# Kernel tuning notes

Hardware: AMD Instinct MI355X
Metric: run time of the kernel (lower is better)

## Reference

```python
import jax, jax.numpy as jnp
import numpy as np

N_NODES = 50000
N_EDGES = 1250000
D_IN = 64
D_HID = 64
D_OUT = 16
N_GRAPHS = 128


def setup_inputs() -> dict:
    key = jax.random.key(0)
    ks = jax.random.split(key, 16)
    glorot = lambda k, shape: jax.random.normal(k, shape, jnp.float32) * (2.0 / (shape[0] + shape[1])) ** 0.5
    inp = {
        "x": jax.random.normal(ks[0], (N_NODES, D_IN), jnp.float32),
        "edge_index": jax.random.randint(ks[1], (2, N_EDGES), 0, N_NODES, jnp.int32),
        "adj": jnp.zeros((1,), jnp.float32),
        "batch": jnp.sort(jax.random.randint(ks[2], (N_NODES,), 0, N_GRAPHS, jnp.int32)),
        # GraphConv layer 1: lin_rel (with bias) on aggregated msgs, lin_root (no bias) on x
        "W_rel1": glorot(ks[3], (D_IN, D_HID)),
        "b_rel1": jnp.zeros((D_HID,), jnp.float32),
        "W_root1": glorot(ks[4], (D_IN, D_HID)),
        "W_rel2": glorot(ks[5], (D_HID, D_HID)),
        "b_rel2": jnp.zeros((D_HID,), jnp.float32),
        "W_root2": glorot(ks[6], (D_HID, D_HID)),
        "W_rel3": glorot(ks[7], (D_HID, D_HID)),
        "b_rel3": jnp.zeros((D_HID,), jnp.float32),
        "W_root3": glorot(ks[8], (D_HID, D_HID)),
        "W_lin": glorot(ks[9], (D_HID, D_OUT)),
        "b_lin": jnp.zeros((D_OUT,), jnp.float32),
    }
    return inp


def graph_conv(x, src, dst, W_rel, b_rel, W_root):
    # PyG GraphConv (aggr='add'): out[i] = (sum_{j->i} x[j]) @ W_rel + b_rel + x[i] @ W_root
    agg = jax.ops.segment_sum(x[src], dst, num_segments=N_NODES)  # [N, d]
    return agg @ W_rel + b_rel + x @ W_root


def reference(x, edge_index, adj, batch,
              W_rel1, b_rel1, W_root1,
              W_rel2, b_rel2, W_root2,
              W_rel3, b_rel3, W_root3,
              W_lin, b_lin):
    src, dst = edge_index[0], edge_index[1]
    h = jax.nn.relu(graph_conv(x, src, dst, W_rel1, b_rel1, W_root1))
    h = jax.nn.relu(graph_conv(h, src, dst, W_rel2, b_rel2, W_root2))
    h = graph_conv(h, src, dst, W_rel3, b_rel3, W_root3)
    # global_mean_pool over batch ids
    sums = jax.ops.segment_sum(h, batch, num_segments=N_GRAPHS)  # [G, d]
    counts = jax.ops.segment_sum(jnp.ones((h.shape[0],), h.dtype), batch, num_segments=N_GRAPHS)
    pooled = sums / jnp.maximum(counts, 1.0)[:, None]
    return pooled @ W_lin + b_lin  # [G, D_OUT]
```

## Files before the change

### kernel.cpp

```cpp
#include <hip/hip_runtime.h>

#define D 64
#define N_GRAPHS 128
#define D_OUT 16
#define BCAP 16384
#define TILE 4096
#define ECAP 2048

typedef unsigned short u16;
typedef unsigned int u32;
typedef unsigned char u8;
typedef __attribute__((ext_vector_type(8))) short bf16x8;
typedef __attribute__((ext_vector_type(4))) float f32x4;
typedef __attribute__((ext_vector_type(2))) float f32x2;

__device__ inline u16 f2bf(float f) {
  u32 u = __float_as_uint(f);
  return (u16)((u + 0x7fffu + ((u >> 16) & 1u)) >> 16);
}
__device__ inline float bf2f(u16 b) { return __uint_as_float((u32)b << 16); }
__device__ inline f32x2 bfpair(u32 v) {
  return (f32x2){__uint_as_float(v << 16), __uint_as_float(v & 0xffff0000u)};
}

__global__ __launch_bounds__(256) void cvtbin_kernel(
    const float* __restrict__ xin, u16* __restrict__ hX, int n4, int nbin,
    const int* __restrict__ src, const int* __restrict__ dst,
    int* __restrict__ cursors, u32* __restrict__ binned, int n_edges, int nbuck,
    const float* __restrict__ Wrel1, const float* __restrict__ Wroot1,
    const float* __restrict__ Wrel2, const float* __restrict__ Wroot2,
    const float* __restrict__ Wrel3, const float* __restrict__ Wroot3,
    const float* __restrict__ Wlin, const float* __restrict__ brel3,
    const float* __restrict__ blin,
    float* __restrict__ M1, float* __restrict__ M2, float* __restrict__ cvec,
    u16* __restrict__ WbT1r, u16* __restrict__ WbT1o,
    u16* __restrict__ WbT2r, u16* __restrict__ WbT2o) {
  __shared__ u32 ent[TILE];
  __shared__ u8 ebk[TILE];
  __shared__ int hist[256];
  __shared__ int startb[256];
  __shared__ int cur[256];
  __shared__ int gbase[256];
  int t = threadIdx.x;

  if ((int)blockIdx.x < nbin) {
    hist[t] = 0;
    __syncthreads();
    int base = blockIdx.x * TILE;
    int cnt = n_edges - base;
    if (cnt > TILE) cnt = TILE;

    int mys[16], myd[16];
#pragma unroll
    for (int j = 0; j < 16; j++) {
      int i = base + t + j * 256;
      if (t + j * 256 < cnt) {
        mys[j] = src[i];
        myd[j] = dst[i];
        atomicAdd(&hist[myd[j] >> 8], 1);
      } else {
        myd[j] = -1;
      }
    }
    __syncthreads();
    int myc = hist[t];
    for (int off = 1; off < 256; off <<= 1) {
      int tmp = (t >= off) ? hist[t - off] : 0;
      __syncthreads();
      hist[t] += tmp;
      __syncthreads();
    }
    int excl = hist[t] - myc;
    startb[t] = excl;
    cur[t] = excl;
    __syncthreads();

#pragma unroll
    for (int j = 0; j < 16; j++) {
      if (myd[j] >= 0) {
        int b = myd[j] >> 8;
        int p = atomicAdd(&cur[b], 1);
        ent[p] = ((u32)myd[j] << 16) | (u32)mys[j];
        ebk[p] = (u8)b;
      }
    }
    __syncthreads();

    if (t < nbuck && myc > 0) gbase[t] = atomicAdd(&cursors[t], myc);
    __syncthreads();

#pragma unroll
    for (int j = 0; j < 16; j++) {
      int p = t + j * 256;
      if (p < cnt) {
        int b = ebk[p];
        int gpos = gbase[b] + (p - startb[b]);
        if (gpos < BCAP) binned[(size_t)b * BCAP + gpos] = ent[p];
      }
    }
    return;
  }

  int cb = blockIdx.x - nbin;
  if (cb == 0) {
    if (t >= 240) {
      int o = t - 240;
      float c = blin[o];
#pragma unroll
      for (int j = 0; j < D; j++) c = fmaf(brel3[j], Wlin[j * D_OUT + o], c);
      cvec[o] = c;
    }
  } else if (cb <= 8) {
    int idx = (cb - 1) * 256 + t;
    const float* W = (idx < 1024) ? Wrel3 : Wroot3;
    float* M = (idx < 1024) ? M1 : M2;
    int id = idx & 1023;
    int k = id >> 4, o = id & 15;
    float acc = 0.0f;
#pragma unroll
    for (int j = 0; j < D; j++) acc = fmaf(W[k * D + j], Wlin[j * D_OUT + o], acc);
    M[id] = acc;
  } else if (cb <= 16) {
    int tid = (cb - 9) * 256 + t;
    int mat = tid >> 9;
    int r = tid & 511;
    int o = r >> 3;
    int k0 = (r & 7) * 8;
    const float* Wsrc = (mat == 0) ? Wrel1 : (mat == 1) ? Wroot1
                       : (mat == 2) ? Wrel2 : Wroot2;
    u16* Wdst = (mat == 0) ? WbT1r : (mat == 1) ? WbT1o
               : (mat == 2) ? WbT2r : WbT2o;
    u16 tmp[8];
#pragma unroll
    for (int j = 0; j < 8; j++) tmp[j] = f2bf(Wsrc[(k0 + j) * D + o]);
    uint4 pw;
    pw.x = (u32)tmp[0] | ((u32)tmp[1] << 16);
    pw.y = (u32)tmp[2] | ((u32)tmp[3] << 16);
    pw.z = (u32)tmp[4] | ((u32)tmp[5] << 16);
    pw.w = (u32)tmp[6] | ((u32)tmp[7] << 16);
    *(uint4*)&Wdst[o * D + k0] = pw;
  }
  int i = cb * 256 + t;
  if (i >= n4) return;
  float4 v = ((const float4*)xin)[i];
  ushort4 o4;
  o4.x = f2bf(v.x); o4.y = f2bf(v.y); o4.z = f2bf(v.z); o4.w = f2bf(v.w);
  ((ushort4*)hX)[i] = o4;
}

__global__ __launch_bounds__(256) void csr_kernel(
    const u32* __restrict__ binned, const int* __restrict__ cursors,
    u16* __restrict__ csr_src, int* __restrict__ offsets,
    int n_nodes, int nbuck) {
  __shared__ int deg[256];
  __shared__ int cur[256];
  __shared__ int red[256];
  __shared__ u16 lcsr[BCAP];
  int b = blockIdx.x, t = threadIdx.x;
  int cnt = cursors[b];
  if (cnt < 0) cnt = 0;
  if (cnt > BCAP) cnt = BCAP;

  int c = 0;
  if (t < b) {
    c = cursors[t];
    if (c < 0) c = 0;
    if (c > BCAP) c = BCAP;
  }
  red[t] = c;
  __syncthreads();
  for (int off = 128; off > 0; off >>= 1) {
    if (t < off) red[t] += red[t + off];
    __syncthreads();
  }
  int ebase = red[0];

  int nodeBase = b << 8;
  int nn = n_nodes - nodeBase;
  if (nn > 256) nn = 256;

  deg[t] = 0;
  __syncthreads();
  const u32* be = binned + (size_t)b * BCAP;
  for (int i = t; i < cnt; i += 256)
    atomicAdd(&deg[(be[i] >> 16) - nodeBase], 1);
  __syncthreads();
  int myd = deg[t];
  for (int off = 1; off < 256; off <<= 1) {
    int tmp = (t >= off) ? deg[t - off] : 0;
    __syncthreads();
    deg[t] += tmp;
    __syncthreads();
  }
  int loff = deg[t] - myd;
  cur[t] = loff;
  if (t < nn) offsets[nodeBase + t] = ebase + loff;
  if (b == nbuck - 1 && t == 0) offsets[n_nodes] = ebase + cnt;
  __syncthreads();

  for (int i = t; i < cnt; i += 256) {
    u32 e = be[i];
    int ln = (e >> 16) - nodeBase;
    int p = atomicAdd(&cur[ln], 1);
    lcsr[p] = (u16)(e & 0xffffu);
  }
  __syncthreads();
  for (int i = t; i < cnt; i += 256) csr_src[ebase + i] = lcsr[i];
}

#define ACC8(a, r) \
  a[0] += bfpair(r.x); a[1] += bfpair(r.y); a[2] += bfpair(r.z); a[3] += bfpair(r.w);

#define GATHER_PROLOGUE(soff, permAr, eidx, blockBase, n_nodes, offsets, csr_src, gsrc, ebase0, scnt) \
  {                                                                     \
    int t_ = threadIdx.x;                                               \
    if (t_ < 33) {                                                      \
      int idx = blockBase + t_;                                         \
      if (idx > n_nodes) idx = n_nodes;                                 \
      soff[t_] = offsets[idx];                                          \
    }                                                                   \
    __syncthreads();                                                    \
    ebase0 = soff[0];                                                   \
    int ecnt_ = soff[32] - ebase0;                                      \
    scnt = ecnt_ < ECAP ? ecnt_ : ECAP;                                 \
    gsrc = csr_src + ebase0;                                            \
    if (t_ < 32) {                                                      \
      int d_ = (blockBase + t_ < n_nodes) ? soff[t_ + 1] - soff[t_] : -1; \
      int r_ = 0;                                                       \
      for (int j_ = 0; j_ < 32; j_++) {                                 \
        int dj_ = (blockBase + j_ < n_nodes) ? soff[j_ + 1] - soff[j_] : -1; \
        if (dj_ > d_ || (dj_ == d_ && j_ < t_)) r_++;                   \
      }                                                                 \
      permAr[r_] = (u8)t_;                                              \
    }                                                                   \
    for (int e_ = t_; e_ < scnt; e_ += 256) eidx[e_] = gsrc[e_];        \
    __syncthreads();                                                    \
  }

#define IDX(i) ((i) < ECAP ? (int)eidx[i] : (int)gsrc[i])

#define GATHER_LOOP(h, fo, ls, le, a0, a1)                                   \
  {                                                                          \
    int i = ls;                                                              \
    for (; i + 7 < le; i += 8) {                                             \
      int s0 = IDX(i),     s1 = IDX(i + 1), s2 = IDX(i + 2), s3 = IDX(i + 3);\
      int s4 = IDX(i + 4), s5 = IDX(i + 5), s6 = IDX(i + 6), s7 = IDX(i + 7);\
      uint4 r0 = *(const uint4*)(h + ((size_t)s0 << 6) + fo);                \
      uint4 r1 = *(const uint4*)(h + ((size_t)s1 << 6) + fo);                \
      uint4 r2 = *(const uint4*)(h + ((size_t)s2 << 6) + fo);                \
      uint4 r3 = *(const uint4*)(h + ((size_t)s3 << 6) + fo);                \
      uint4 r4 = *(const uint4*)(h + ((size_t)s4 << 6) + fo);                \
      uint4 r5 = *(const uint4*)(h + ((size_t)s5 << 6) + fo);                \
      uint4 r6 = *(const uint4*)(h + ((size_t)s6 << 6) + fo);                \
      uint4 r7 = *(const uint4*)(h + ((size_t)s7 << 6) + fo);                \
      ACC8(a0, r0) ACC8(a1, r1) ACC8(a0, r2) ACC8(a1, r3)                    \
      ACC8(a0, r4) ACC8(a1, r5) ACC8(a0, r6) ACC8(a1, r7)                    \
    }                                                                        \
    for (; i + 3 < le; i += 4) {                                             \
      int s0 = IDX(i), s1 = IDX(i + 1), s2 = IDX(i + 2), s3 = IDX(i + 3);    \
      uint4 r0 = *(const uint4*)(h + ((size_t)s0 << 6) + fo);                \
      uint4 r1 = *(const uint4*)(h + ((size_t)s1 << 6) + fo);                \
      uint4 r2 = *(const uint4*)(h + ((size_t)s2 << 6) + fo);                \
      uint4 r3 = *(const uint4*)(h + ((size_t)s3 << 6) + fo);                \
      ACC8(a0, r0) ACC8(a1, r1) ACC8(a0, r2) ACC8(a1, r3)                    \
    }                                                                        \
    for (; i < le; i++) {                                                    \
      int s0 = IDX(i);                                                       \
      uint4 r0 = *(const uint4*)(h + ((size_t)s0 << 6) + fo);                \
      ACC8(a0, r0)                                                           \
    }                                                                        \
  }

__global__ __launch_bounds__(256) void fused_layer_kernel(
    const u16* __restrict__ h, const int* __restrict__ offsets,
    const u16* __restrict__ csr_src,
    const u16* __restrict__ WbTrel, const u16* __restrict__ WbTroot,
    const float* __restrict__ brel,
    u16* __restrict__ h_out, int n_nodes, int do_relu) {
  __shared__ __align__(16) u16 ldsA[32 * 72];
  __shared__ __align__(16) u16 ldsX[32 * 72];
  __shared__ int soff[33];
  __shared__ u8 permAr[32];
  __shared__ u16 eidx[ECAP];
  int w = threadIdx.x >> 6;
  int lane = threadIdx.x & 63;
  int sub = lane >> 3;
  int fo = (lane & 7) * 8;
  int blockBase = blockIdx.x * 32;
  const u16* gsrc;
  int ebase0, scnt;

  GATHER_PROLOGUE(soff, permAr, eidx, blockBase, n_nodes, offsets, csr_src, gsrc, ebase0, scnt)

  int ln = permAr[w * 8 + sub];
  int node = blockBase + ln;
  bool valid = node < n_nodes;
  int ls = soff[ln] - ebase0;
  int le = soff[ln + 1] - ebase0;
  if (!valid) le = ls;
  int lrow = ln * 72;

  uint4 xr = make_uint4(0, 0, 0, 0);
  if (valid) xr = *(const uint4*)(h + ((size_t)node << 6) + fo);
  *(uint4*)&ldsX[lrow + fo] = xr;

  f32x2 a0[4] = {{0,0},{0,0},{0,0},{0,0}};
  f32x2 a1[4] = {{0,0},{0,0},{0,0},{0,0}};
  GATHER_LOOP(h, fo, ls, le, a0, a1)
#pragma unroll
  for (int k = 0; k < 4; k++) a0[k] += a1[k];

  uint4 pa;
  pa.x = (u32)f2bf(a0[0].x) | ((u32)f2bf(a0[0].y) << 16);
  pa.y = (u32)f2bf(a0[1].x) | ((u32)f2bf(a0[1].y) << 16);
  pa.z = (u32)f2bf(a0[2].x) | ((u32)f2bf(a0[2].y) << 16);
  pa.w = (u32)f2bf(a0[3].x) | ((u32)f2bf(a0[3].y) << 16);
  *(uint4*)&ldsA[lrow + fo] = pa;
  __syncthreads();

  int mt = w & 1;
  int ntb = (w >> 1) * 2;
  int lr = lane & 15, lk = lane >> 4;
  int arow = (mt * 16 + lr) * 72;
  bf16x8 af0 = *(const bf16x8*)&ldsA[arow + lk * 8];
  bf16x8 af1 = *(const bf16x8*)&ldsA[arow + 32 + lk * 8];
  bf16x8 xf0 = *(const bf16x8*)&ldsX[arow + lk * 8];
  bf16x8 xf1 = *(const bf16x8*)&ldsX[arow + 32 + lk * 8];
#pragma unroll
  for (int tt = 0; tt < 2; tt++) {
    int nt = ntb + tt;
    int wrow = (nt * 16 + lr) * D + lk * 8;
    bf16x8 br0 = *(const bf16x8*)(WbTrel + wrow);
    bf16x8 br1 = *(const bf16x8*)(WbTrel + wrow + 32);
    bf16x8 bo0 = *(const bf16x8*)(WbTroot + wrow);
    bf16x8 bo1 = *(const bf16x8*)(WbTroot + wrow + 32);
    f32x4 acc = {0.0f, 0.0f, 0.0f, 0.0f};
    acc = __builtin_amdgcn_mfma_f32_16x16x32_bf16(af0, br0, acc, 0, 0, 0);
    acc = __builtin_amdgcn_mfma_f32_16x16x32_bf16(af1, br1, acc, 0, 0, 0);
    acc = __builtin_amdgcn_mfma_f32_16x16x32_bf16(xf0, bo0, acc, 0, 0, 0);
    acc = __builtin_amdgcn_mfma_f32_16x16x32_bf16(xf1, bo1, acc, 0, 0, 0);
    float bias = brel[nt * 16 + lr];
#pragma unroll
    for (int r = 0; r < 4; r++) {
      int onode = blockBase + mt * 16 + lk * 4 + r;
      if (onode < n_nodes) {
        float v = acc[r] + bias;
        if (do_relu) v = fmaxf(v, 0.0f);
        h_out[((size_t)onode << 6) + nt * 16 + lr] = f2bf(v);
      }
    }
  }
}

__global__ __launch_bounds__(256) void gather_pool_kernel(
    const u16* __restrict__ h, const int* __restrict__ offsets,
    const u16* __restrict__ csr_src, const int* __restrict__ batch,
    float* __restrict__ pooledA, float* __restrict__ pooledH, int n_nodes) {
  __shared__ int soff[33];
  __shared__ u8 permAr[32];
  __shared__ u16 eidx[ECAP];
  __shared__ int gid[32];
  __shared__ float ldsPA[32][D];
  __shared__ float ldsPH[32][D];
  int w = threadIdx.x >> 6;
  int lane = threadIdx.x & 63;
  int sub = lane >> 3;
  int fo = (lane & 7) * 8;
  int blockBase = blockIdx.x * 32;
  if (threadIdx.x < 32)
    gid[threadIdx.x] = (blockBase + threadIdx.x < n_nodes) ? batch[blockBase + threadIdx.x] : -1;
  const u16* gsrc;
  int ebase0, scnt;

  GATHER_PROLOGUE(soff, permAr, eidx, blockBase, n_nodes, offsets, csr_src, gsrc, ebase0, scnt)

  int ln = permAr[w * 8 + sub];
  int node = blockBase + ln;
  bool valid = node < n_nodes;
  int ls = soff[ln] - ebase0;
  int le = soff[ln + 1] - ebase0;
  if (!valid) le = ls;

  f32x2 a0[4] = {{0,0},{0,0},{0,0},{0,0}};
  f32x2 a1[4] = {{0,0},{0,0},{0,0},{0,0}};
  GATHER_LOOP(h, fo, ls, le, a0, a1)
#pragma unroll
  for (int k = 0; k < 4; k++) a0[k] += a1[k];

  uint4 xr = make_uint4(0, 0, 0, 0);
  if (valid) xr = *(const uint4*)(h + ((size_t)node << 6) + fo);
  f32x2 x0 = bfpair(xr.x), x1 = bfpair(xr.y), x2 = bfpair(xr.z), x3 = bfpair(xr.w);
  float* rowA = &ldsPA[ln][fo];
  float* rowH = &ldsPH[ln][fo];
  rowA[0] = a0[0].x; rowA[1] = a0[0].y; rowA[2] = a0[1].x; rowA[3] = a0[1].y;
  rowA[4] = a0[2].x; rowA[5] = a0[2].y; rowA[6] = a0[3].x; rowA[7] = a0[3].y;
  rowH[0] = x0.x; rowH[1] = x0.y; rowH[2] = x1.x; rowH[3] = x1.y;
  rowH[4] = x2.x; rowH[5] = x2.y; rowH[6] = x3.x; rowH[7] = x3.y;
  __syncthreads();

  if (threadIdx.x < 128) {
    int half = threadIdx.x >> 6;
    int f = threadIdx.x & 63;
    float* dst = half ? pooledH : pooledA;
    float acc = 0.0f;
    int curg = -1;
#pragma unroll 1
    for (int n = 0; n < 32; n++) {
      int g = gid[n];
      if (g < 0) break;
      float v = half ? ldsPH[n][f] : ldsPA[n][f];
      if (g != curg) {
        if (curg >= 0) atomicAdd(dst + curg * D + f, acc);
        curg = g;
        acc = v;
      } else {
        acc += v;
      }
    }
    if (curg >= 0) atomicAdd(dst + curg * D + f, acc);
  }
}

__global__ __launch_bounds__(64) void final_kernel(
    const float* __restrict__ pooledA, const float* __restrict__ pooledH,
    const float* __restrict__ M1, const float* __restrict__ M2,
    const float* __restrict__ cvec, const float* __restrict__ blin,
    const int* __restrict__ batch, float* __restrict__ out, int n_nodes) {
  __shared__ int seg[2];
  int g = blockIdx.x;
  int t = threadIdx.x;
  if (t < 2) {
    int target = g + t;
    int lo = 0, hi = n_nodes;
    while (lo < hi) {
      int mid = (lo + hi) >> 1;
      if (batch[mid] < target) lo = mid + 1; else hi = mid;
    }
    seg[t] = lo;
  }
  __syncthreads();
  int cnt = seg[1] - seg[0];
  if (t < D_OUT) {
    float res;
    if (cnt > 0) {
      float inv = 1.0f / (float)cnt;
      float acc = cvec[t];
#pragma unroll
      for (int k = 0; k < D; k++)
        acc = fmaf(pooledA[g * D + k] * inv, M1[k * D_OUT + t],
              fmaf(pooledH[g * D + k] * inv, M2[k * D_OUT + t], acc));
      res = acc;
    } else {
      res = blin[t];
    }
    out[g * D_OUT + t] = res;
  }
}

extern "C" void kernel_launch(void* const* d_in, const int* in_sizes, int n_in,
                              void* d_out, int out_size, void* d_ws, size_t ws_size,
                              hipStream_t stream) {
  const float* x     = (const float*)d_in[0];
  const int*   ei    = (const int*)d_in[1];
  const int*   batch = (const int*)d_in[3];
  const float* Wrel1 = (const float*)d_in[4];
  const float* brel1 = (const float*)d_in[5];
  const float* Wroot1= (const float*)d_in[6];
  const float* Wrel2 = (const float*)d_in[7];
  const float* brel2 = (const float*)d_in[8];
  const float* Wroot2= (const float*)d_in[9];
  const float* Wrel3 = (const float*)d_in[10];
  const float* brel3 = (const float*)d_in[11];
  const float* Wroot3= (const float*)d_in[12];
  const float* Wlin  = (const float*)d_in[13];
  const float* blin  = (const float*)d_in[14];
  float* out = (float*)d_out;

  const int n_edges = in_sizes[1] / 2;
  const int n_nodes = in_sizes[0] / D;
  const int* src = ei;
  const int* dst = ei + n_edges;
  const int nbuck = (n_nodes + 255) >> 8;

  char* p = (char*)d_ws;
  u32* binned  = (u32*)p;    p += (size_t)nbuck * BCAP * sizeof(u32);
  int* cursors = (int*)p;    p += 256 * sizeof(int);
  float* pooledA = (float*)p; p += (size_t)N_GRAPHS * D * sizeof(float);
  float* pooledH = (float*)p; p += (size_t)N_GRAPHS * D * sizeof(float);
  float* M1     = (float*)p; p += (size_t)D * D_OUT * sizeof(float);
  float* M2     = (float*)p; p += (size_t)D * D_OUT * sizeof(float);
  float* cvec   = (float*)p; p += 16 * sizeof(float);
  int* offsets  = (int*)p;   p += (size_t)(n_nodes + 4) * sizeof(int);
  u16* hX       = (u16*)p;   p += (size_t)n_nodes * D * sizeof(u16);
  u16* h1       = (u16*)p;   p += (size_t)n_nodes * D * sizeof(u16);
  u16* h2       = (u16*)p;   p += (size_t)n_nodes * D * sizeof(u16);
  u16* csr_src  = (u16*)p;   p += (size_t)n_edges * sizeof(u16);
  u16* WbT1r    = (u16*)p;   p += (size_t)D * D * sizeof(u16);
  u16* WbT1o    = (u16*)p;   p += (size_t)D * D * sizeof(u16);
  u16* WbT2r    = (u16*)p;   p += (size_t)D * D * sizeof(u16);
  u16* WbT2o    = (u16*)p;   p += (size_t)D * D * sizeof(u16);

  const int bin_blocks = (n_edges + TILE - 1) / TILE;
  const int cvt_n4 = n_nodes * D / 4;
  const int cvt_blocks = (cvt_n4 + 255) / 256;
  const int fused_blocks = (n_nodes + 31) / 32;

  const size_t zero_bytes = 256 * sizeof(int) + 2 * (size_t)N_GRAPHS * D * sizeof(float);
  hipMemsetAsync(cursors, 0, zero_bytes, stream);

  cvtbin_kernel<<<bin_blocks + cvt_blocks, 256, 0, stream>>>(
      x, hX, cvt_n4, bin_blocks, src, dst, cursors, binned, n_edges, nbuck,
      Wrel1, Wroot1, Wrel2, Wroot2, Wrel3, Wroot3, Wlin, brel3, blin,
      M1, M2, cvec, WbT1r, WbT1o, WbT2r, WbT2o);
  csr_kernel<<<nbuck, 256, 0, stream>>>(binned, cursors, csr_src, offsets, n_nodes, nbuck);

  fused_layer_kernel<<<fused_blocks, 256, 0, stream>>>(
      hX, offsets, csr_src, WbT1r, WbT1o, brel1, h1, n_nodes, 1);
  fused_layer_kernel<<<fused_blocks, 256, 0, stream>>>(
      h1, offsets, csr_src, WbT2r, WbT2o, brel2, h2, n_nodes, 1);

  gather_pool_kernel<<<fused_blocks, 256, 0, stream>>>(
      h2, offsets, csr_src, batch, pooledA, pooledH, n_nodes);

  final_kernel<<<N_GRAPHS, 64, 0, stream>>>(
      pooledA, pooledH, M1, M2, cvec, blin, batch, out, n_nodes);
}
```

Before: 228.3 us.

## Split neighbor gather into two feature halves separated by a grid-wide soft barrier

The gather in the fused layer and pool kernels now reads 8-byte half-rows: all blocks first accumulate features 0-31, meet at a spin-wait global barrier with a timeout, then accumulate features 32-63. The goal is to halve the working set of the random gather at any one time so that the 3.2 MB half of the feature table stays in cache. The cost is smaller per-load transactions, twice the index traversal, and a grid-wide spin barrier. With 1563 blocks not all co-resident, the barrier can only finish through its timeout, which may add long stalls.

```diff
diff --git a/kernel.cpp b/kernel.cpp
--- a/kernel.cpp
+++ b/kernel.cpp
@@ -207,9 +207,6 @@
   __syncthreads();
   for (int i = t; i < cnt; i += 256) csr_src[ebase + i] = lcsr[i];
 }
-
-#define ACC8(a, r) \
-  a[0] += bfpair(r.x); a[1] += bfpair(r.y); a[2] += bfpair(r.z); a[3] += bfpair(r.w);
 
 #define GATHER_PROLOGUE(soff, permAr, eidx, blockBase, n_nodes, offsets, csr_src, gsrc, ebase0, scnt) \
   {                                                                     \
@@ -239,44 +236,61 @@
 
 #define IDX(i) ((i) < ECAP ? (int)eidx[i] : (int)gsrc[i])
 
-#define GATHER_LOOP(h, fo, ls, le, a0, a1)                                   \
+#define ACC4(a, r) a[0] += bfpair(r.x); a[1] += bfpair(r.y);
+
+#define GATHER_LOOP_HALF(h, eoff, ls, le, a0, a1)                            \
   {                                                                          \
     int i = ls;                                                              \
     for (; i + 7 < le; i += 8) {                                             \
       int s0 = IDX(i),     s1 = IDX(i + 1), s2 = IDX(i + 2), s3 = IDX(i + 3);\
       int s4 = IDX(i + 4), s5 = IDX(i + 5), s6 = IDX(i + 6), s7 = IDX(i + 7);\
-      uint4 r0 = *(const uint4*)(h + ((size_t)s0 << 6) + fo);                \
-      uint4 r1 = *(const uint4*)(h + ((size_t)s1 << 6) + fo);                \
-      uint4 r2 = *(const uint4*)(h + ((size_t)s2 << 6) + fo);                \
-      uint4 r3 = *(const uint4*)(h + ((size_t)s3 << 6) + fo);                \
-      uint4 r4 = *(const uint4*)(h + ((size_t)s4 << 6) + fo);                \
-      uint4 r5 = *(const uint4*)(h + ((size_t)s5 << 6) + fo);                \
-      uint4 r6 = *(const uint4*)(h + ((size_t)s6 << 6) + fo);                \
-      uint4 r7 = *(const uint4*)(h + ((size_t)s7 << 6) + fo);                \
-      ACC8(a0, r0) ACC8(a1, r1) ACC8(a0, r2) ACC8(a1, r3)                    \
-      ACC8(a0, r4) ACC8(a1, r5) ACC8(a0, r6) ACC8(a1, r7)                    \
+      uint2 r0 = *(const uint2*)(h + ((size_t)s0 << 6) + (eoff));            \
+      uint2 r1 = *(const uint2*)(h + ((size_t)s1 << 6) + (eoff));            \
+      uint2 r2 = *(const uint2*)(h + ((size_t)s2 << 6) + (eoff));            \
+      uint2 r3 = *(const uint2*)(h + ((size_t)s3 << 6) + (eoff));            \
+      uint2 r4 = *(const uint2*)(h + ((size_t)s4 << 6) + (eoff));            \
+      uint2 r5 = *(const uint2*)(h + ((size_t)s5 << 6) + (eoff));            \
+      uint2 r6 = *(const uint2*)(h + ((size_t)s6 << 6) + (eoff));            \
+      uint2 r7 = *(const uint2*)(h + ((size_t)s7 << 6) + (eoff));            \
+      ACC4(a0, r0) ACC4(a1, r1) ACC4(a0, r2) ACC4(a1, r3)                    \
+      ACC4(a0, r4) ACC4(a1, r5) ACC4(a0, r6) ACC4(a1, r7)                    \
     }                                                                        \
     for (; i + 3 < le; i += 4) {                                             \
       int s0 = IDX(i), s1 = IDX(i + 1), s2 = IDX(i + 2), s3 = IDX(i + 3);    \
-      uint4 r0 = *(const uint4*)(h + ((size_t)s0 << 6) + fo);                \
-      uint4 r1 = *(const uint4*)(h + ((size_t)s1 << 6) + fo);                \
-      uint4 r2 = *(const uint4*)(h + ((size_t)s2 << 6) + fo);                \
-      uint4 r3 = *(const uint4*)(h + ((size_t)s3 << 6) + fo);                \
-      ACC8(a0, r0) ACC8(a1, r1) ACC8(a0, r2) ACC8(a1, r3)                    \
+      uint2 r0 = *(const uint2*)(h + ((size_t)s0 << 6) + (eoff));            \
+      uint2 r1 = *(const uint2*)(h + ((size_t)s1 << 6) + (eoff));            \
+      uint2 r2 = *(const uint2*)(h + ((size_t)s2 << 6) + (eoff));            \
+      uint2 r3 = *(const uint2*)(h + ((size_t)s3 << 6) + (eoff));            \
+      ACC4(a0, r0) ACC4(a1, r1) ACC4(a0, r2) ACC4(a1, r3)                    \
     }                                                                        \
     for (; i < le; i++) {                                                    \
       int s0 = IDX(i);                                                       \
-      uint4 r0 = *(const uint4*)(h + ((size_t)s0 << 6) + fo);                \
-      ACC8(a0, r0)                                                           \
+      uint2 r0 = *(const uint2*)(h + ((size_t)s0 << 6) + (eoff));            \
+      ACC4(a0, r0)                                                           \
     }                                                                        \
   }
+
+__device__ inline void soft_barrier(int* ctr, int nblk) {
+  __syncthreads();
+  if (threadIdx.x == 0) {
+    atomicAdd(ctr, 1);
+    int spins = 0;
+    while (__hip_atomic_load(ctr, __ATOMIC_ACQUIRE, __HIP_MEMORY_SCOPE_AGENT) < nblk
+           && spins < 20000) {
+      __builtin_amdgcn_s_sleep(64);
+      spins++;
+    }
+  }
+  __syncthreads();
+}
 
 __global__ __launch_bounds__(256) void fused_layer_kernel(
     const u16* __restrict__ h, const int* __restrict__ offsets,
     const u16* __restrict__ csr_src,
     const u16* __restrict__ WbTrel, const u16* __restrict__ WbTroot,
     const float* __restrict__ brel,
-    u16* __restrict__ h_out, int n_nodes, int do_relu) {
+    u16* __restrict__ h_out, int n_nodes, int do_relu,
+    int* __restrict__ bctr, int nblk) {
   __shared__ __align__(16) u16 ldsA[32 * 72];
   __shared__ __align__(16) u16 ldsX[32 * 72];
   __shared__ int soff[33];
@@ -285,7 +299,7 @@
   int w = threadIdx.x >> 6;
   int lane = threadIdx.x & 63;
   int sub = lane >> 3;
-  int fo = (lane & 7) * 8;
+  int flane = lane & 7;
   int blockBase = blockIdx.x * 32;
   const u16* gsrc;
   int ebase0, scnt;
@@ -300,22 +314,31 @@
   if (!valid) le = ls;
   int lrow = ln * 72;
 
-  uint4 xr = make_uint4(0, 0, 0, 0);
-  if (valid) xr = *(const uint4*)(h + ((size_t)node << 6) + fo);
-  *(uint4*)&ldsX[lrow + fo] = xr;
-
-  f32x2 a0[4] = {{0,0},{0,0},{0,0},{0,0}};
-  f32x2 a1[4] = {{0,0},{0,0},{0,0},{0,0}};
-  GATHER_LOOP(h, fo, ls, le, a0, a1)
-#pragma unroll
-  for (int k = 0; k < 4; k++) a0[k] += a1[k];
-
-  uint4 pa;
-  pa.x = (u32)f2bf(a0[0].x) | ((u32)f2bf(a0[0].y) << 16);
-  pa.y = (u32)f2bf(a0[1].x) | ((u32)f2bf(a0[1].y) << 16);
-  pa.z = (u32)f2bf(a0[2].x) | ((u32)f2bf(a0[2].y) << 16);
-  pa.w = (u32)f2bf(a0[3].x) | ((u32)f2bf(a0[3].y) << 16);
-  *(uint4*)&ldsA[lrow + fo] = pa;
+  uint2 xr0 = make_uint2(0, 0);
+  if (valid) xr0 = *(const uint2*)(h + ((size_t)node << 6) + flane * 4);
+  *(uint2*)&ldsX[lrow + flane * 4] = xr0;
+
+  f32x2 a0[2] = {{0,0},{0,0}}, a1[2] = {{0,0},{0,0}};
+  GATHER_LOOP_HALF(h, flane * 4, ls, le, a0, a1)
+  a0[0] += a1[0]; a0[1] += a1[1];
+  uint2 pa0;
+  pa0.x = (u32)f2bf(a0[0].x) | ((u32)f2bf(a0[0].y) << 16);
+  pa0.y = (u32)f2bf(a0[1].x) | ((u32)f2bf(a0[1].y) << 16);
+  *(uint2*)&ldsA[lrow + flane * 4] = pa0;
+
+  soft_barrier(bctr, nblk);
+
+  uint2 xr1 = make_uint2(0, 0);
+  if (valid) xr1 = *(const uint2*)(h + ((size_t)node << 6) + 32 + flane * 4);
+  *(uint2*)&ldsX[lrow + 32 + flane * 4] = xr1;
+
+  f32x2 b0[2] = {{0,0},{0,0}}, b1[2] = {{0,0},{0,0}};
+  GATHER_LOOP_HALF(h, 32 + flane * 4, ls, le, b0, b1)
+  b0[0] += b1[0]; b0[1] += b1[1];
+  uint2 pa1;
+  pa1.x = (u32)f2bf(b0[0].x) | ((u32)f2bf(b0[0].y) << 16);
+  pa1.y = (u32)f2bf(b0[1].x) | ((u32)f2bf(b0[1].y) << 16);
+  *(uint2*)&ldsA[lrow + 32 + flane * 4] = pa1;
   __syncthreads();
 
   int mt = w & 1;
@@ -355,7 +378,8 @@
 __global__ __launch_bounds__(256) void gather_pool_kernel(
     const u16* __restrict__ h, const int* __restrict__ offsets,
     const u16* __restrict__ csr_src, const int* __restrict__ batch,
-    float* __restrict__ pooledA, float* __restrict__ pooledH, int n_nodes) {
+    float* __restrict__ pooledA, float* __restrict__ pooledH, int n_nodes,
+    int* __restrict__ bctr, int nblk) {
   __shared__ int soff[33];
   __shared__ u8 permAr[32];
   __shared__ u16 eidx[ECAP];
@@ -365,7 +389,7 @@
   int w = threadIdx.x >> 6;
   int lane = threadIdx.x & 63;
   int sub = lane >> 3;
-  int fo = (lane & 7) * 8;
+  int flane = lane & 7;
   int blockBase = blockIdx.x * 32;
   if (threadIdx.x < 32)
     gid[threadIdx.x] = (blockBase + threadIdx.x < n_nodes) ? batch[blockBase + threadIdx.x] : -1;
@@ -381,21 +405,33 @@
   int le = soff[ln + 1] - ebase0;
   if (!valid) le = ls;
 
-  f32x2 a0[4] = {{0,0},{0,0},{0,0},{0,0}};
-  f32x2 a1[4] = {{0,0},{0,0},{0,0},{0,0}};
-  GATHER_LOOP(h, fo, ls, le, a0, a1)
-#pragma unroll
-  for (int k = 0; k < 4; k++) a0[k] += a1[k];
-
-  uint4 xr = make_uint4(0, 0, 0, 0);
-  if (valid) xr = *(const uint4*)(h + ((size_t)node << 6) + fo);
-  f32x2 x0 = bfpair(xr.x), x1 = bfpair(xr.y), x2 = bfpair(xr.z), x3 = bfpair(xr.w);
-  float* rowA = &ldsPA[ln][fo];
-  float* rowH = &ldsPH[ln][fo];
-  rowA[0] = a0[0].x; rowA[1] = a0[0].y; rowA[2] = a0[1].x; rowA[3] = a0[1].y;
-  rowA[4] = a0[2].x; rowA[5] = a0[2].y; rowA[6] = a0[3].x; rowA[7] = a0[3].y;
-  rowH[0] = x0.x; rowH[1] = x0.y; rowH[2] = x1.x; rowH[3] = x1.y;
-  rowH[4] = x2.x; rowH[5] = x2.y; rowH[6] = x3.x; rowH[7] = x3.y;
+  uint2 xr0 = make_uint2(0, 0);
+  if (valid) xr0 = *(const uint2*)(h + ((size_t)node << 6) + flane * 4);
+  f32x2 a0[2] = {{0,0},{0,0}}, a1[2] = {{0,0},{0,0}};
+  GATHER_LOOP_HALF(h, flane * 4, ls, le, a0, a1)
+  a0[0] += a1[0]; a0[1] += a1[1];
+  {
+    f32x2 x0 = bfpair(xr0.x), x1 = bfpair(xr0.y);
+    float* rowA = &ldsPA[ln][flane * 4];
+    float* rowH = &ldsPH[ln][flane * 4];
+    rowA[0] = a0[0].x; rowA[1] = a0[0].y; rowA[2] = a0[1].x; rowA[3] = a0[1].y;
+    rowH[0] = x0.x; rowH[1] = x0.y; rowH[2] = x1.x; rowH[3] = x1.y;
+  }
+
+  soft_barrier(bctr, nblk);
+
+  uint2 xr1 = make_uint2(0, 0);
+  if (valid) xr1 = *(const uint2*)(h + ((size_t)node << 6) + 32 + flane * 4);
+  f32x2 b0[2] = {{0,0},{0,0}}, b1[2] = {{0,0},{0,0}};
+  GATHER_LOOP_HALF(h, 32 + flane * 4, ls, le, b0, b1)
+  b0[0] += b1[0]; b0[1] += b1[1];
+  {
+    f32x2 x0 = bfpair(xr1.x), x1 = bfpair(xr1.y);
+    float* rowA = &ldsPA[ln][32 + flane * 4];
+    float* rowH = &ldsPH[ln][32 + flane * 4];
+    rowA[0] = b0[0].x; rowA[1] = b0[0].y; rowA[2] = b0[1].x; rowA[3] = b0[1].y;
+    rowH[0] = x0.x; rowH[1] = x0.y; rowH[2] = x1.x; rowH[3] = x1.y;
+  }
   __syncthreads();
 
   if (threadIdx.x < 128) {
@@ -487,6 +523,7 @@
   int* cursors = (int*)p;    p += 256 * sizeof(int);
   float* pooledA = (float*)p; p += (size_t)N_GRAPHS * D * sizeof(float);
   float* pooledH = (float*)p; p += (size_t)N_GRAPHS * D * sizeof(float);
+  int* bctr    = (int*)p;    p += 4 * sizeof(int);
   float* M1     = (float*)p; p += (size_t)D * D_OUT * sizeof(float);
   float* M2     = (float*)p; p += (size_t)D * D_OUT * sizeof(float);
   float* cvec   = (float*)p; p += 16 * sizeof(float);
@@ -505,7 +542,8 @@
   const int cvt_blocks = (cvt_n4 + 255) / 256;
   const int fused_blocks = (n_nodes + 31) / 32;
 
-  const size_t zero_bytes = 256 * sizeof(int) + 2 * (size_t)N_GRAPHS * D * sizeof(float);
+  const size_t zero_bytes = 256 * sizeof(int)
+      + 2 * (size_t)N_GRAPHS * D * sizeof(float) + 4 * sizeof(int);
   hipMemsetAsync(cursors, 0, zero_bytes, stream);
 
   cvtbin_kernel<<<bin_blocks + cvt_blocks, 256, 0, stream>>>(
@@ -515,12 +553,15 @@
   csr_kernel<<<nbuck, 256, 0, stream>>>(binned, cursors, csr_src, offsets, n_nodes, nbuck);
 
   fused_layer_kernel<<<fused_blocks, 256, 0, stream>>>(
-      hX, offsets, csr_src, WbT1r, WbT1o, brel1, h1, n_nodes, 1);
+      hX, offsets, csr_src, WbT1r, WbT1o, brel1, h1, n_nodes, 1,
+      bctr + 0, fused_blocks);
   fused_layer_kernel<<<fused_blocks, 256, 0, stream>>>(
-      h1, offsets, csr_src, WbT2r, WbT2o, brel2, h2, n_nodes, 1);
+      h1, offsets, csr_src, WbT2r, WbT2o, brel2, h2, n_nodes, 1,
+      bctr + 1, fused_blocks);
 
   gather_pool_kernel<<<fused_blocks, 256, 0, stream>>>(
-      h2, offsets, csr_src, batch, pooledA, pooledH, n_nodes);
+      h2, offsets, csr_src, batch, pooledA, pooledH, n_nodes,
+      bctr + 2, fused_blocks);
 
   final_kernel<<<N_GRAPHS, 64, 0, stream>>>(
       pooledA, pooledH, M1, M2, cvec, blin, batch, out, n_nodes);
```

Result: slower. 880.2 us (+285.6%).

## Split each node's CSR neighbor list by source half for locality

Applied to the files above, without the earlier changes.

The CSR build now counts and places each node's incoming edges in two groups, sources below and above n_nodes/2, and records a per-node midpoint offset. The gather kernels walk the low-source group first and then the high-source group. The aim is to make concurrent wavefronts touch a narrower slice of the feature table at a time, improving L2 hit rates. The 8-way unrolled gather loop is removed, which lowers memory-level parallelism per thread, and an extra midpoint array plus more per-node logic are added.

```diff
diff --git a/kernel.cpp b/kernel.cpp
--- a/kernel.cpp
+++ b/kernel.cpp
@@ -151,9 +151,9 @@
 __global__ __launch_bounds__(256) void csr_kernel(
     const u32* __restrict__ binned, const int* __restrict__ cursors,
     u16* __restrict__ csr_src, int* __restrict__ offsets,
-    int n_nodes, int nbuck) {
-  __shared__ int deg[256];
-  __shared__ int cur[256];
+    int* __restrict__ midoff, int n_nodes, int nbuck, int halfThresh) {
+  __shared__ int deg2[512];
+  __shared__ int cur2[512];
   __shared__ int red[256];
   __shared__ u16 lcsr[BCAP];
   int b = blockIdx.x, t = threadIdx.x;
@@ -179,29 +179,42 @@
   int nn = n_nodes - nodeBase;
   if (nn > 256) nn = 256;
 
-  deg[t] = 0;
+  deg2[t] = 0;
+  deg2[t + 256] = 0;
   __syncthreads();
   const u32* be = binned + (size_t)b * BCAP;
-  for (int i = t; i < cnt; i += 256)
-    atomicAdd(&deg[(be[i] >> 16) - nodeBase], 1);
-  __syncthreads();
-  int myd = deg[t];
-  for (int off = 1; off < 256; off <<= 1) {
-    int tmp = (t >= off) ? deg[t - off] : 0;
-    __syncthreads();
-    deg[t] += tmp;
-    __syncthreads();
-  }
-  int loff = deg[t] - myd;
-  cur[t] = loff;
-  if (t < nn) offsets[nodeBase + t] = ebase + loff;
-  if (b == nbuck - 1 && t == 0) offsets[n_nodes] = ebase + cnt;
-  __syncthreads();
-
   for (int i = t; i < cnt; i += 256) {
     u32 e = be[i];
     int ln = (e >> 16) - nodeBase;
-    int p = atomicAdd(&cur[ln], 1);
+    int half = ((int)(e & 0xffffu) >= halfThresh) ? 1 : 0;
+    atomicAdd(&deg2[ln * 2 + half], 1);
+  }
+  __syncthreads();
+  int lowc = deg2[t * 2], highc = deg2[t * 2 + 1];
+  int myTotal = lowc + highc;
+  red[t] = myTotal;
+  __syncthreads();
+  for (int off = 1; off < 256; off <<= 1) {
+    int tmp = (t >= off) ? red[t - off] : 0;
+    __syncthreads();
+    red[t] += tmp;
+    __syncthreads();
+  }
+  int excl = red[t] - myTotal;
+  cur2[t * 2] = excl;
+  cur2[t * 2 + 1] = excl + lowc;
+  if (t < nn) {
+    offsets[nodeBase + t] = ebase + excl;
+    midoff[nodeBase + t] = ebase + excl + lowc;
+  }
+  if (b == nbuck - 1 && t == 0) offsets[n_nodes] = ebase + cnt;
+  __syncthreads();
+
+  for (int i = t; i < cnt; i += 256) {
+    u32 e = be[i];
+    int ln = (e >> 16) - nodeBase;
+    int half = ((int)(e & 0xffffu) >= halfThresh) ? 1 : 0;
+    int p = atomicAdd(&cur2[ln * 2 + half], 1);
     lcsr[p] = (u16)(e & 0xffffu);
   }
   __syncthreads();
@@ -211,13 +224,18 @@
 #define ACC8(a, r) \
   a[0] += bfpair(r.x); a[1] += bfpair(r.y); a[2] += bfpair(r.z); a[3] += bfpair(r.w);
 
-#define GATHER_PROLOGUE(soff, permAr, eidx, blockBase, n_nodes, offsets, csr_src, gsrc, ebase0, scnt) \
+#define GATHER_PROLOGUE(soff, smid, permAr, eidx, blockBase, n_nodes, offsets, midoff, csr_src, gsrc, ebase0, scnt) \
   {                                                                     \
     int t_ = threadIdx.x;                                               \
     if (t_ < 33) {                                                      \
       int idx = blockBase + t_;                                         \
       if (idx > n_nodes) idx = n_nodes;                                 \
       soff[t_] = offsets[idx];                                          \
+    }                                                                   \
+    if (t_ >= 64 && t_ < 96) {                                          \
+      int n_ = t_ - 64;                                                 \
+      int idx = blockBase + n_;                                         \
+      smid[n_] = (idx < n_nodes) ? midoff[idx] : 0;                     \
     }                                                                   \
     __syncthreads();                                                    \
     ebase0 = soff[0];                                                   \
@@ -242,20 +260,6 @@
 #define GATHER_LOOP(h, fo, ls, le, a0, a1)                                   \
   {                                                                          \
     int i = ls;                                                              \
-    for (; i + 7 < le; i += 8) {                                             \
-      int s0 = IDX(i),     s1 = IDX(i + 1), s2 = IDX(i + 2), s3 = IDX(i + 3);\
-      int s4 = IDX(i + 4), s5 = IDX(i + 5), s6 = IDX(i + 6), s7 = IDX(i + 7);\
-      uint4 r0 = *(const uint4*)(h + ((size_t)s0 << 6) + fo);                \
-      uint4 r1 = *(const uint4*)(h + ((size_t)s1 << 6) + fo);                \
-      uint4 r2 = *(const uint4*)(h + ((size_t)s2 << 6) + fo);                \
-      uint4 r3 = *(const uint4*)(h + ((size_t)s3 << 6) + fo);                \
-      uint4 r4 = *(const uint4*)(h + ((size_t)s4 << 6) + fo);                \
-      uint4 r5 = *(const uint4*)(h + ((size_t)s5 << 6) + fo);                \
-      uint4 r6 = *(const uint4*)(h + ((size_t)s6 << 6) + fo);                \
-      uint4 r7 = *(const uint4*)(h + ((size_t)s7 << 6) + fo);                \
-      ACC8(a0, r0) ACC8(a1, r1) ACC8(a0, r2) ACC8(a1, r3)                    \
-      ACC8(a0, r4) ACC8(a1, r5) ACC8(a0, r6) ACC8(a1, r7)                    \
-    }                                                                        \
     for (; i + 3 < le; i += 4) {                                             \
       int s0 = IDX(i), s1 = IDX(i + 1), s2 = IDX(i + 2), s3 = IDX(i + 3);    \
       uint4 r0 = *(const uint4*)(h + ((size_t)s0 << 6) + fo);                \
@@ -273,13 +277,14 @@
 
 __global__ __launch_bounds__(256) void fused_layer_kernel(
     const u16* __restrict__ h, const int* __restrict__ offsets,
-    const u16* __restrict__ csr_src,
+    const int* __restrict__ midoff, const u16* __restrict__ csr_src,
     const u16* __restrict__ WbTrel, const u16* __restrict__ WbTroot,
     const float* __restrict__ brel,
     u16* __restrict__ h_out, int n_nodes, int do_relu) {
   __shared__ __align__(16) u16 ldsA[32 * 72];
   __shared__ __align__(16) u16 ldsX[32 * 72];
   __shared__ int soff[33];
+  __shared__ int smid[32];
   __shared__ u8 permAr[32];
   __shared__ u16 eidx[ECAP];
   int w = threadIdx.x >> 6;
@@ -290,7 +295,7 @@
   const u16* gsrc;
   int ebase0, scnt;
 
-  GATHER_PROLOGUE(soff, permAr, eidx, blockBase, n_nodes, offsets, csr_src, gsrc, ebase0, scnt)
+  GATHER_PROLOGUE(soff, smid, permAr, eidx, blockBase, n_nodes, offsets, midoff, csr_src, gsrc, ebase0, scnt)
 
   int ln = permAr[w * 8 + sub];
   int node = blockBase + ln;
@@ -298,6 +303,9 @@
   int ls = soff[ln] - ebase0;
   int le = soff[ln + 1] - ebase0;
   if (!valid) le = ls;
+  int lm = valid ? smid[ln] - ebase0 : ls;
+  if (lm < ls) lm = ls;
+  if (lm > le) lm = le;
   int lrow = ln * 72;
 
   uint4 xr = make_uint4(0, 0, 0, 0);
@@ -306,7 +314,8 @@
 
   f32x2 a0[4] = {{0,0},{0,0},{0,0},{0,0}};
   f32x2 a1[4] = {{0,0},{0,0},{0,0},{0,0}};
-  GATHER_LOOP(h, fo, ls, le, a0, a1)
+  GATHER_LOOP(h, fo, ls, lm, a0, a1)
+  GATHER_LOOP(h, fo, lm, le, a0, a1)
 #pragma unroll
   for (int k = 0; k < 4; k++) a0[k] += a1[k];
 
@@ -354,9 +363,11 @@
 
 __global__ __launch_bounds__(256) void gather_pool_kernel(
     const u16* __restrict__ h, const int* __restrict__ offsets,
-    const u16* __restrict__ csr_src, const int* __restrict__ batch,
+    const int* __restrict__ midoff, const u16* __restrict__ csr_src,
+    const int* __restrict__ batch,
     float* __restrict__ pooledA, float* __restrict__ pooledH, int n_nodes) {
   __shared__ int soff[33];
+  __shared__ int smid[32];
   __shared__ u8 permAr[32];
   __shared__ u16 eidx[ECAP];
   __shared__ int gid[32];
@@ -372,7 +383,7 @@
   const u16* gsrc;
   int ebase0, scnt;
 
-  GATHER_PROLOGUE(soff, permAr, eidx, blockBase, n_nodes, offsets, csr_src, gsrc, ebase0, scnt)
+  GATHER_PROLOGUE(soff, smid, permAr, eidx, blockBase, n_nodes, offsets, midoff, csr_src, gsrc, ebase0, scnt)
 
   int ln = permAr[w * 8 + sub];
   int node = blockBase + ln;
@@ -380,10 +391,14 @@
   int ls = soff[ln] - ebase0;
   int le = soff[ln + 1] - ebase0;
   if (!valid) le = ls;
+  int lm = valid ? smid[ln] - ebase0 : ls;
+  if (lm < ls) lm = ls;
+  if (lm > le) lm = le;
 
   f32x2 a0[4] = {{0,0},{0,0},{0,0},{0,0}};
   f32x2 a1[4] = {{0,0},{0,0},{0,0},{0,0}};
-  GATHER_LOOP(h, fo, ls, le, a0, a1)
+  GATHER_LOOP(h, fo, ls, lm, a0, a1)
+  GATHER_LOOP(h, fo, lm, le, a0, a1)
 #pragma unroll
   for (int k = 0; k < 4; k++) a0[k] += a1[k];
 
@@ -481,6 +496,7 @@
   const int* src = ei;
   const int* dst = ei + n_edges;
   const int nbuck = (n_nodes + 255) >> 8;
+  const int halfThresh = n_nodes / 2;
 
   char* p = (char*)d_ws;
   u32* binned  = (u32*)p;    p += (size_t)nbuck * BCAP * sizeof(u32);
@@ -491,6 +507,7 @@
   float* M2     = (float*)p; p += (size_t)D * D_OUT * sizeof(float);
   float* cvec   = (float*)p; p += 16 * sizeof(float);
   int* offsets  = (int*)p;   p += (size_t)(n_nodes + 4) * sizeof(int);
+  int* midoff   = (int*)p;   p += (size_t)(n_nodes + 4) * sizeof(int);
   u16* hX       = (u16*)p;   p += (size_t)n_nodes * D * sizeof(u16);
   u16* h1       = (u16*)p;   p += (size_t)n_nodes * D * sizeof(u16);
   u16* h2       = (u16*)p;   p += (size_t)n_nodes * D * sizeof(u16);
@@ -512,15 +529,16 @@
       x, hX, cvt_n4, bin_blocks, src, dst, cursors, binned, n_edges, nbuck,
       Wrel1, Wroot1, Wrel2, Wroot2, Wrel3, Wroot3, Wlin, brel3, blin,
       M1, M2, cvec, WbT1r, WbT1o, WbT2r, WbT2o);
-  csr_kernel<<<nbuck, 256, 0, stream>>>(binned, cursors, csr_src, offsets, n_nodes, nbuck);
+  csr_kernel<<<nbuck, 256, 0, stream>>>(
+      binned, cursors, csr_src, offsets, midoff, n_nodes, nbuck, halfThresh);
 
   fused_layer_kernel<<<fused_blocks, 256, 0, stream>>>(
-      hX, offsets, csr_src, WbT1r, WbT1o, brel1, h1, n_nodes, 1);
+      hX, offsets, midoff, csr_src, WbT1r, WbT1o, brel1, h1, n_nodes, 1);
   fused_layer_kernel<<<fused_blocks, 256, 0, stream>>>(
-      h1, offsets, csr_src, WbT2r, WbT2o, brel2, h2, n_nodes, 1);
+      h1, offsets, midoff, csr_src, WbT2r, WbT2o, brel2, h2, n_nodes, 1);
 
   gather_pool_kernel<<<fused_blocks, 256, 0, stream>>>(
-      h2, offsets, csr_src, batch, pooledA, pooledH, n_nodes);
+      h2, offsets, midoff, csr_src, batch, pooledA, pooledH, n_nodes);
 
   final_kernel<<<N_GRAPHS, 64, 0, stream>>>(
       pooledA, pooledH, M1, M2, cvec, blin, batch, out, n_nodes);
```

New measurement: 219.3 us (median of 2 runs). 1.04x faster.
